# Optimization experiments

Hardware: AMD Instinct MI355X
Metric: run time of the kernel (lower is better)

## Reference

```python
import jax, jax.numpy as jnp
import numpy as np

# Model dims
B, S, H = 1, 1024, 2048
NH, NKV, DH = 32, 8, 64
G = NH // NKV            # GQA group size
E, K, I = 8, 2, 2048     # experts, top_k, intermediate
ALPHA, LIMIT = 1.702, 7.0
EPS = 1e-5
SCALE = DH ** -0.5


def rmsnorm(x, g):
    return x * jax.lax.rsqrt(jnp.mean(x * x, axis=-1, keepdims=True) + EPS) * g


def setup_inputs() -> dict:
    key = jax.random.key(0)
    ks = jax.random.split(key, 24)
    w = lambda k, shp: jax.random.normal(k, shp, dtype=jnp.float32) * 0.02
    causal = jnp.where(jnp.tril(jnp.ones((S, S), dtype=bool)), 0.0, -1e9).astype(jnp.float32)
    return {
        "hidden_states": jax.random.normal(ks[0], (B, S, H), dtype=jnp.float32),
        "attention_bias": causal[None, None, :, :],           # [1,1,S,S]
        "ln1_g": jnp.ones((H,), jnp.float32),
        "ln2_g": jnp.ones((H,), jnp.float32),
        "Wq": w(ks[1], (NH * DH, H)),  "bq": w(ks[2], (NH * DH,)),
        "Wk": w(ks[3], (NKV * DH, H)), "bk": w(ks[4], (NKV * DH,)),
        "Wv": w(ks[5], (NKV * DH, H)), "bv": w(ks[6], (NKV * DH,)),
        "Wo": w(ks[7], (H, NH * DH)),  "bo": w(ks[8], (H,)),
        "sinks": w(ks[9], (NH,)),
        "router_w": w(ks[10], (E, H)), "router_b": w(ks[11], (E,)),
        "We_gate": w(ks[12], (E, I, H)), "be_gate": w(ks[13], (E, I)),
        "We_up":   w(ks[14], (E, I, H)), "be_up":   w(ks[15], (E, I)),
        "We_down": w(ks[16], (E, H, I)), "be_down": w(ks[17], (E, H)),
    }


def reference(hidden_states, attention_bias, ln1_g, ln2_g,
              Wq, bq, Wk, bk, Wv, bv, Wo, bo, sinks,
              router_w, router_b,
              We_gate, be_gate, We_up, be_up, We_down, be_down):
    x = hidden_states
    # ---- pre-norm sink attention ----
    xn = rmsnorm(x, ln1_g)
    q = (xn @ Wq.T + bq).reshape(B, S, NH, DH).transpose(0, 2, 1, 3)    # [B,NH,S,DH]
    k = (xn @ Wk.T + bk).reshape(B, S, NKV, DH).transpose(0, 2, 1, 3)   # [B,NKV,S,DH]
    v = (xn @ Wv.T + bv).reshape(B, S, NKV, DH).transpose(0, 2, 1, 3)
    # GQA: replicate each kv head G times consecutively (repeat_kv)
    k = jnp.repeat(k, G, axis=1)
    v = jnp.repeat(v, G, axis=1)
    scores = jnp.einsum('bhqd,bhkd->bhqk', q, k) * SCALE + attention_bias  # [B,NH,S,S]
    sink_col = jnp.broadcast_to(sinks.reshape(1, NH, 1, 1), (B, NH, S, 1))
    combined = jnp.concatenate([scores, sink_col], axis=-1)               # [B,NH,S,S+1]
    probs = jax.nn.softmax(combined, axis=-1)[..., :-1]                   # drop sink
    attn = jnp.einsum('bhqk,bhkd->bhqd', probs, v)
    attn = attn.transpose(0, 2, 1, 3).reshape(B, S, NH * DH)
    h = x + (attn @ Wo.T + bo)
    # ---- pre-norm MoE FFN ----
    hn = rmsnorm(h, ln2_g)
    router_logits = hn @ router_w.T + router_b                            # [B,S,E]
    rw, sel = jax.lax.top_k(router_logits, K)
    rw = jax.nn.softmax(rw, axis=-1)                                      # [B,S,K]
    # dense per-expert MLP over all tokens (matches the exported loop)
    gate = jnp.einsum('bsh,eih->bsei', hn, We_gate) + be_gate             # [B,S,E,I]
    up = jnp.einsum('bsh,eih->bsei', hn, We_up) + be_up
    gate_c = jnp.minimum(gate, LIMIT)
    up_c = jnp.clip(up, -LIMIT, LIMIT)
    glu = gate_c * jax.nn.sigmoid(ALPHA * gate_c)
    gated = (up_c + 1.0) * glu
    down = jnp.einsum('bsei,ehi->bseh', gated, We_down) + be_down         # [B,S,E,H]
    # per-token expert weight: sum_k rw * (sel == e)
    wts = jnp.sum(rw[..., None] * (sel[..., None] == jnp.arange(E)), axis=2)  # [B,S,E]
    moe = jnp.einsum('bseh,bse->bsh', down, wts)
    return h + moe
```

## Files before the change

### kernel.cpp

```cpp
#include <hip/hip_runtime.h>
#include <hip/hip_bf16.h>

#define HD 2048
#define SEQ 1024
#define NHEAD 32
#define NKVH 8
#define DHEAD 64
#define NEXP 8
#define INTER 2048
#define SCALE 0.125f
#define ALPHA 1.702f
#define LIMIT 7.0f

typedef __attribute__((ext_vector_type(8))) short short8;
typedef __attribute__((ext_vector_type(4))) short short4v;
typedef __attribute__((ext_vector_type(4))) float f32x4;

__device__ __forceinline__ unsigned short f2bf(float f) {
  union { float f; unsigned u; } v; v.f = f;
  unsigned r = v.u + 0x7fffu + ((v.u >> 16) & 1u);
  return (unsigned short)(r >> 16);
}
__device__ __forceinline__ float bf2f(unsigned short h) {
  union { unsigned u; float f; } v; v.u = ((unsigned)h) << 16; return v.f;
}
__device__ __forceinline__ void split2(float f, unsigned short& hi, unsigned short& lo) {
  hi = f2bf(f);
  lo = f2bf(f - bf2f(hi));
}

__device__ __forceinline__ f32x4 mfma32(short8 a, short8 b, f32x4 c) {
  return __builtin_amdgcn_mfma_f32_16x16x32_bf16(a, b, c, 0, 0, 0);
}

__device__ __forceinline__ void gl_lds16(const float* g, float* l) {
  __builtin_amdgcn_global_load_lds(
      (const __attribute__((address_space(1))) unsigned int*)g,
      (__attribute__((address_space(3))) unsigned int*)l, 16, 0, 0);
}

__global__ __launch_bounds__(256) void rmsnorm_split_kernel(
    const float* __restrict__ x, const float* __restrict__ gamma,
    unsigned short* __restrict__ oh, unsigned short* __restrict__ ol) {
  int row = blockIdx.x, tid = threadIdx.x;
  const float* xr = x + (size_t)row * HD;
  float v[8];
#pragma unroll
  for (int i = 0; i < 8; ++i) v[i] = xr[tid * 8 + i];
  float ss = 0.f;
#pragma unroll
  for (int i = 0; i < 8; ++i) ss += v[i] * v[i];
#pragma unroll
  for (int off = 32; off; off >>= 1) ss += __shfl_xor(ss, off, 64);
  __shared__ float wss[4];
  if ((tid & 63) == 0) wss[tid >> 6] = ss;
  __syncthreads();
  float rs = rsqrtf((wss[0] + wss[1] + wss[2] + wss[3]) * (1.0f / HD) + 1e-5f);
  short8 vh, vl;
#pragma unroll
  for (int i = 0; i < 8; ++i) {
    float val = v[i] * rs * gamma[tid * 8 + i];
    unsigned short h, lo;
    split2(val, h, lo);
    vh[i] = (short)h;
    vl[i] = (short)lo;
  }
  *(short8*)(oh + (size_t)row * HD + tid * 8) = vh;
  *(short8*)(ol + (size_t)row * HD + tid * 8) = vl;
}

__global__ __launch_bounds__(256) void rmsnorm_plain_kernel(
    const float* __restrict__ x, const float* __restrict__ gamma,
    unsigned short* __restrict__ out) {
  int row = blockIdx.x, tid = threadIdx.x;
  const float* xr = x + (size_t)row * HD;
  float v[8];
#pragma unroll
  for (int i = 0; i < 8; ++i) v[i] = xr[tid * 8 + i];
  float ss = 0.f;
#pragma unroll
  for (int i = 0; i < 8; ++i) ss += v[i] * v[i];
#pragma unroll
  for (int off = 32; off; off >>= 1) ss += __shfl_xor(ss, off, 64);
  __shared__ float wss[4];
  if ((tid & 63) == 0) wss[tid >> 6] = ss;
  __syncthreads();
  float rs = rsqrtf((wss[0] + wss[1] + wss[2] + wss[3]) * (1.0f / HD) + 1e-5f);
  short8 o;
#pragma unroll
  for (int i = 0; i < 8; ++i) o[i] = (short)f2bf(v[i] * rs * gamma[tid * 8 + i]);
  *(short8*)(out + (size_t)row * HD + tid * 8) = o;
}

template <int MT, int NS, bool SPLIT, int EPI>
__global__ __launch_bounds__(512) void gemm_gl(
    const unsigned short* __restrict__ Ah, const unsigned short* __restrict__ Al,
    int ldA,
    const float* __restrict__ W0, const float* __restrict__ W1,
    const float* __restrict__ W2,
    const float* __restrict__ b0, const float* __restrict__ b1,
    const float* __restrict__ b2,
    const float* __restrict__ resid,
    const int* __restrict__ counts, const int* __restrict__ arows,
    const int* __restrict__ orows,
    unsigned short* __restrict__ oh0, unsigned short* __restrict__ ol0,
    unsigned short* __restrict__ oh1, unsigned short* __restrict__ ol1,
    unsigned short* __restrict__ oh2, unsigned short* __restrict__ ol2,
    float* __restrict__ f0, float* __restrict__ f1,
    int M, int Kd) {
  constexpr int MG = MT * 16 * 8;
  constexpr int NR = NS * 16;
  constexpr int RPW = NR / 8;
  constexpr int NI = RPW / 4;
  __shared__ __align__(16) float lw[2][NR][64];
  int tid = threadIdx.x, l = tid & 63, w = tid >> 6;
  int g = l >> 4, q = l & 15;
  int n0 = blockIdx.x * NR;

  const float* Wb;
  const float* bias;
  int nloc = n0, e = 0, mat = 0;
  if constexpr (EPI == 0) {
    if (n0 < NHEAD * DHEAD) {
      Wb = W0; bias = b0;
    } else if (n0 < NHEAD * DHEAD + NKVH * DHEAD) {
      Wb = W1; bias = b1; nloc = n0 - NHEAD * DHEAD;
    } else {
      Wb = W2; bias = b2; nloc = n0 - (NHEAD * DHEAD + NKVH * DHEAD);
    }
  } else if constexpr (EPI == 1) {
    Wb = W0; bias = b0;
  } else if constexpr (EPI == 2) {
    e = blockIdx.z >> 1;
    mat = blockIdx.z & 1;
    Wb = (mat ? W1 : W0) + (size_t)e * INTER * HD;
    bias = (mat ? b1 : b0) + (size_t)e * INTER;
  } else {
    e = blockIdx.z;
    Wb = W0 + (size_t)e * HD * INTER;
    bias = b0 + (size_t)e * HD;
  }
  int cnt = (EPI >= 2) ? counts[e] : M;

  const float* sptr[NI];
  float* sdst0[NI];
  float* sdst1[NI];
#pragma unroll
  for (int j = 0; j < NI; ++j) {
    int r = RPW * w + 4 * j + (l >> 4);
    int gs = ((l & 15) ^ (r & 7)) * 4;
    sptr[j] = Wb + (size_t)(nloc + r) * Kd + gs;
    sdst0[j] = &lw[0][RPW * w + 4 * j][0];
    sdst1[j] = &lw[1][RPW * w + 4 * j][0];
  }
  auto stage = [&](int buf, int kc) {
#pragma unroll
    for (int j = 0; j < NI; ++j)
      gl_lds16(sptr[j] + kc, buf ? sdst1[j] : sdst0[j]);
  };

  int mstart = (EPI <= 1) ? blockIdx.y : 0;
  int mstep = (EPI <= 1) ? gridDim.y : 1;

  for (int mg = mstart; mg * MG < cnt; mg += mstep) {
    int mb = mg * MG + w * (MT * 16);
    const unsigned short* ap[MT];
    const unsigned short* apl[MT];
#pragma unroll
    for (int mt = 0; mt < MT; ++mt) {
      int mm = min(mb + mt * 16 + q, cnt - 1);
      int ar = (EPI >= 2) ? arows[e * SEQ + mm] : mm;
      ap[mt] = Ah + (size_t)ar * ldA + 8 * g;
      if constexpr (SPLIT) apl[mt] = Al + (size_t)ar * ldA + 8 * g;
    }
    f32x4 acc[MT][NS];
#pragma unroll
    for (int mt = 0; mt < MT; ++mt)
#pragma unroll
      for (int ns = 0; ns < NS; ++ns) acc[mt][ns] = (f32x4){0.f, 0.f, 0.f, 0.f};

    stage(0, 0);
    short8 ab[2][MT], abl[2][MT];
#pragma unroll
    for (int mt = 0; mt < MT; ++mt) {
      ab[0][mt] = *(const short8*)(ap[mt]);
      ab[1][mt] = *(const short8*)(ap[mt] + 32);
      if constexpr (SPLIT) {
        abl[0][mt] = *(const short8*)(apl[mt]);
        abl[1][mt] = *(const short8*)(apl[mt] + 32);
      }
    }
    __syncthreads();

    int nc = Kd / 64;
    for (int c = 0; c < nc; ++c) {
      int u = c & 1;
      if (c + 1 < nc) stage(u ^ 1, (c + 1) * 64);
#pragma unroll
      for (int kh = 0; kh < 2; ++kh) {
        short8 acur[MT], acl[MT];
#pragma unroll
        for (int mt = 0; mt < MT; ++mt) {
          acur[mt] = ab[kh][mt];
          if constexpr (SPLIT) acl[mt] = abl[kh][mt];
        }
        int kn = c * 64 + kh * 32 + 64;
        if (kn < Kd) {
#pragma unroll
          for (int mt = 0; mt < MT; ++mt) {
            ab[kh][mt] = *(const short8*)(ap[mt] + kn);
            if constexpr (SPLIT) abl[kh][mt] = *(const short8*)(apl[mt] + kn);
          }
        }
        short8 wh[NS], wl[NS];
#pragma unroll
        for (int ns = 0; ns < NS; ++ns) {
          int row = ns * 16 + q;
          int r7 = q & 7;
          int i0 = ((kh * 8 + g * 2) ^ r7) * 16;
          int i1 = ((kh * 8 + g * 2 + 1) ^ r7) * 16;
          const char* base = (const char*)&lw[u][row][0];
          float4 v0 = *(const float4*)(base + i0);
          float4 v1 = *(const float4*)(base + i1);
          float vv[8] = {v0.x, v0.y, v0.z, v0.w, v1.x, v1.y, v1.z, v1.w};
#pragma unroll
          for (int jj = 0; jj < 8; ++jj) {
            if constexpr (SPLIT) {
              unsigned short h, lo;
              split2(vv[jj], h, lo);
              wh[ns][jj] = (short)h;
              wl[ns][jj] = (short)lo;
            } else {
              wh[ns][jj] = (short)f2bf(vv[jj]);
            }
          }
        }
#pragma unroll
        for (int mt = 0; mt < MT; ++mt)
#pragma unroll
          for (int ns = 0; ns < NS; ++ns) {
            acc[mt][ns] = mfma32(acur[mt], wh[ns], acc[mt][ns]);
            if constexpr (SPLIT) {
              acc[mt][ns] = mfma32(acur[mt], wl[ns], acc[mt][ns]);
              acc[mt][ns] = mfma32(acl[mt], wh[ns], acc[mt][ns]);
            }
          }
      }
      __syncthreads();
    }
#pragma unroll
    for (int ns = 0; ns < NS; ++ns) {
      int ncol = nloc + ns * 16 + q;
      float bs = bias[ncol];
#pragma unroll
      for (int mt = 0; mt < MT; ++mt) {
#pragma unroll
        for (int r = 0; r < 4; ++r) {
          int mr = mb + mt * 16 + 4 * g + r;
          float val = acc[mt][ns][r] + bs;
          if constexpr (EPI == 0) {
            unsigned short h, lo;
            split2(val, h, lo);
            if (n0 < NHEAD * DHEAD) {
              oh0[(size_t)mr * (NHEAD * DHEAD) + ncol] = h;
              ol0[(size_t)mr * (NHEAD * DHEAD) + ncol] = lo;
            } else if (n0 < NHEAD * DHEAD + NKVH * DHEAD) {
              oh1[(size_t)mr * (NKVH * DHEAD) + ncol] = h;
              ol1[(size_t)mr * (NKVH * DHEAD) + ncol] = lo;
            } else {
              oh2[(size_t)ncol * SEQ + mr] = h;
              ol2[(size_t)ncol * SEQ + mr] = lo;
            }
          } else if constexpr (EPI == 1) {
            f0[(size_t)mr * HD + ncol] = val + resid[(size_t)mr * HD + ncol];
          } else if constexpr (EPI == 2) {
            if (mr < cnt) {
              int slot = orows[e * SEQ + mr];
              (mat ? f1 : f0)[(size_t)slot * INTER + ncol] = val;
            }
          } else {
            if (mr < cnt) {
              int slot = orows[e * SEQ + mr];
              f0[(size_t)slot * HD + ncol] = val;
            }
          }
        }
      }
    }
  }
}

__global__ __launch_bounds__(256) void attn_kernel(
    const unsigned short* __restrict__ Qh, const unsigned short* __restrict__ Ql,
    const unsigned short* __restrict__ Kh, const unsigned short* __restrict__ Kl,
    const unsigned short* __restrict__ Vh, const unsigned short* __restrict__ Vl,
    const float* __restrict__ sinks, unsigned short* __restrict__ outh,
    unsigned short* __restrict__ outl) {
  __shared__ __align__(16) unsigned short pbuf[4][2][16][40];
  int l = threadIdx.x & 63, widx = threadIdx.x >> 6;
  int wid = blockIdx.x * 4 + widx;
  int head = wid >> 6, qt = wid & 63;
  int q0 = qt * 16;
  int g = l >> 4, q = l & 15;
  int kvh = head >> 2;
  size_t qoff = (size_t)(q0 + q) * (NHEAD * DHEAD) + head * DHEAD + 8 * g;
  short8 qh0 = *(const short8*)(Qh + qoff);
  short8 qh1 = *(const short8*)(Qh + qoff + 32);
  short8 ql0 = *(const short8*)(Ql + qoff);
  short8 ql1 = *(const short8*)(Ql + qoff + 32);
  float m = sinks[head];
  float lsum = 1.0f;
  f32x4 o[4] = {{0, 0, 0, 0}, {0, 0, 0, 0}, {0, 0, 0, 0}, {0, 0, 0, 0}};
  int qglob = q0 + q;
  for (int kt = 0; kt <= qt; kt += 2) {
    bool hasB = (kt + 1) <= qt;
    size_t koff = (size_t)(kt * 16 + q) * (NKVH * DHEAD) + kvh * DHEAD + 8 * g;
    f32x4 stA = {0, 0, 0, 0};
    {
      short8 kh0 = *(const short8*)(Kh + koff);
      short8 kh1 = *(const short8*)(Kh + koff + 32);
      short8 kl0 = *(const short8*)(Kl + koff);
      short8 kl1 = *(const short8*)(Kl + koff + 32);
      stA = mfma32(kh0, qh0, stA);
      stA = mfma32(kh0, ql0, stA);
      stA = mfma32(kl0, qh0, stA);
      stA = mfma32(kh1, qh1, stA);
      stA = mfma32(kh1, ql1, stA);
      stA = mfma32(kl1, qh1, stA);
    }
    f32x4 stB = {0, 0, 0, 0};
    if (hasB) {
      size_t koff2 = koff + (size_t)16 * (NKVH * DHEAD);
      short8 kh0 = *(const short8*)(Kh + koff2);
      short8 kh1 = *(const short8*)(Kh + koff2 + 32);
      short8 kl0 = *(const short8*)(Kl + koff2);
      short8 kl1 = *(const short8*)(Kl + koff2 + 32);
      stB = mfma32(kh0, qh0, stB);
      stB = mfma32(kh0, ql0, stB);
      stB = mfma32(kl0, qh0, stB);
      stB = mfma32(kh1, qh1, stB);
      stB = mfma32(kh1, ql1, stB);
      stB = mfma32(kl1, qh1, stB);
    }
    float sA[4], sB[4];
#pragma unroll
    for (int r = 0; r < 4; ++r) {
      int keyA = kt * 16 + 4 * g + r;
      sA[r] = (keyA <= qglob) ? stA[r] * SCALE : -1e30f;
      sB[r] = (hasB && keyA + 16 <= qglob) ? stB[r] * SCALE : -1e30f;
    }
    float mt = fmaxf(fmaxf(fmaxf(sA[0], sA[1]), fmaxf(sA[2], sA[3])),
                     fmaxf(fmaxf(sB[0], sB[1]), fmaxf(sB[2], sB[3])));
    mt = fmaxf(mt, __shfl_xor(mt, 16, 64));
    mt = fmaxf(mt, __shfl_xor(mt, 32, 64));
    float mnew = fmaxf(m, mt);
    float corr = __expf(m - mnew);
    float pA[4], pB[4];
    float rsum = 0.f;
#pragma unroll
    for (int r = 0; r < 4; ++r) {
      pA[r] = __expf(sA[r] - mnew);
      pB[r] = __expf(sB[r] - mnew);
      rsum += pA[r] + pB[r];
    }
    rsum += __shfl_xor(rsum, 16, 64);
    rsum += __shfl_xor(rsum, 32, 64);
    lsum = lsum * corr + rsum;
    m = mnew;
#pragma unroll
    for (int dt = 0; dt < 4; ++dt)
#pragma unroll
      for (int r = 0; r < 4; ++r) o[dt][r] *= corr;
    unsigned short ph[8], pl[8];
#pragma unroll
    for (int r = 0; r < 4; ++r) {
      split2(pA[r], ph[r], pl[r]);
      split2(pB[r], ph[4 + r], pl[4 + r]);
    }
    short4v wAh = {(short)ph[0], (short)ph[1], (short)ph[2], (short)ph[3]};
    short4v wBh = {(short)ph[4], (short)ph[5], (short)ph[6], (short)ph[7]};
    short4v wAl = {(short)pl[0], (short)pl[1], (short)pl[2], (short)pl[3]};
    short4v wBl = {(short)pl[4], (short)pl[5], (short)pl[6], (short)pl[7]};
    *(short4v*)&pbuf[widx][0][q][4 * g] = wAh;
    *(short4v*)&pbuf[widx][0][q][16 + 4 * g] = wBh;
    *(short4v*)&pbuf[widx][1][q][4 * g] = wAl;
    *(short4v*)&pbuf[widx][1][q][16 + 4 * g] = wBl;
    asm volatile("s_waitcnt lgkmcnt(0)" ::: "memory");
    short8 pbh = *(const short8*)&pbuf[widx][0][q][8 * g];
    short8 pbl = *(const short8*)&pbuf[widx][1][q][8 * g];
    size_t vbase = (size_t)(kvh * DHEAD) * SEQ + kt * 16 + 8 * g;
#pragma unroll
    for (int dt = 0; dt < 4; ++dt) {
      size_t voff = vbase + (size_t)(dt * 16 + q) * SEQ;
      short8 vh8 = *(const short8*)(Vh + voff);
      short8 vl8 = *(const short8*)(Vl + voff);
      o[dt] = mfma32(vh8, pbh, o[dt]);
      o[dt] = mfma32(vh8, pbl, o[dt]);
      o[dt] = mfma32(vl8, pbh, o[dt]);
    }
  }
  float inv = 1.0f / lsum;
#pragma unroll
  for (int dt = 0; dt < 4; ++dt)
#pragma unroll
    for (int r = 0; r < 4; ++r) {
      float val = o[dt][r] * inv;
      unsigned short h, lo;
      split2(val, h, lo);
      size_t idx = (size_t)qglob * (NHEAD * DHEAD) + head * DHEAD + dt * 16 + 4 * g + r;
      outh[idx] = h;
      outl[idx] = lo;
    }
}

__global__ __launch_bounds__(64) void router_kernel(
    const float* __restrict__ h, const float* __restrict__ gamma,
    const float* __restrict__ rw, const float* __restrict__ rb,
    float* __restrict__ wsel, int* __restrict__ counts,
    int* __restrict__ lists, int* __restrict__ slotof) {
  int t = blockIdx.x;
  int l = threadIdx.x;
  const float* hr = h + (size_t)t * HD;
  double ss = 0.0;
  for (int i = l; i < HD; i += 64) {
    double x = (double)hr[i];
    ss += x * x;
  }
#pragma unroll
  for (int off = 32; off; off >>= 1) ss += __shfl_xor(ss, off, 64);
  double rs = rsqrt(ss * (1.0 / HD) + 1e-5);
  double acc[NEXP];
#pragma unroll
  for (int e = 0; e < NEXP; ++e) acc[e] = 0.0;
  for (int i = l; i < HD; i += 64) {
    double xh = (double)hr[i] * rs * (double)gamma[i];
#pragma unroll
    for (int e = 0; e < NEXP; ++e) acc[e] += xh * (double)rw[e * HD + i];
  }
#pragma unroll
  for (int e = 0; e < NEXP; ++e)
#pragma unroll
    for (int off = 32; off; off >>= 1) acc[e] += __shfl_xor(acc[e], off, 64);
  if (l == 0) {
    double lg[NEXP];
#pragma unroll
    for (int e = 0; e < NEXP; ++e) lg[e] = acc[e] + (double)rb[e];
    int e0 = 0;
#pragma unroll
    for (int e = 1; e < NEXP; ++e)
      if (lg[e] > lg[e0]) e0 = e;
    int e1 = -1;
#pragma unroll
    for (int e = 0; e < NEXP; ++e)
      if (e != e0 && (e1 < 0 || lg[e] > lg[e1])) e1 = e;
    double d = exp(lg[e1] - lg[e0]);
    float p0 = (float)(1.0 / (1.0 + d)), p1 = (float)(d / (1.0 + d));
    wsel[2 * t] = p0;
    wsel[2 * t + 1] = p1;
    int s0 = atomicAdd(&counts[e0], 1);
    lists[e0 * SEQ + s0] = t;
    slotof[e0 * SEQ + s0] = 2 * t;
    int s1 = atomicAdd(&counts[e1], 1);
    lists[e1 * SEQ + s1] = t;
    slotof[e1 * SEQ + s1] = 2 * t + 1;
  }
}

__global__ __launch_bounds__(256) void act_kernel(
    const float* __restrict__ rg, const float* __restrict__ ru,
    unsigned short* __restrict__ gated) {
  size_t base = (size_t)blockIdx.x * INTER + threadIdx.x * 8;
  float4 g0 = *(const float4*)(rg + base);
  float4 g1 = *(const float4*)(rg + base + 4);
  float4 u0 = *(const float4*)(ru + base);
  float4 u1 = *(const float4*)(ru + base + 4);
  float gv[8] = {g0.x, g0.y, g0.z, g0.w, g1.x, g1.y, g1.z, g1.w};
  float uv[8] = {u0.x, u0.y, u0.z, u0.w, u1.x, u1.y, u1.z, u1.w};
  short8 o;
#pragma unroll
  for (int j = 0; j < 8; ++j) {
    float gc = fminf(gv[j], LIMIT);
    float uc = fminf(fmaxf(uv[j], -LIMIT), LIMIT);
    float glu = gc / (1.f + __expf(-ALPHA * gc));
    o[j] = (short)f2bf((uc + 1.f) * glu);
  }
  *(short8*)(gated + base) = o;
}

__global__ __launch_bounds__(256) void reduce_kernel(
    const float* __restrict__ hbuf, const float* __restrict__ scr,
    const float* __restrict__ wsel, float* __restrict__ out) {
  int t = blockIdx.x;
  int c = threadIdx.x * 8;
  float w0 = wsel[2 * t], w1 = wsel[2 * t + 1];
  size_t hb = (size_t)t * HD + c;
  size_t s0 = (size_t)(2 * t) * HD + c;
  size_t s1 = (size_t)(2 * t + 1) * HD + c;
#pragma unroll
  for (int j = 0; j < 2; ++j) {
    float4 hv = *(const float4*)(hbuf + hb + 4 * j);
    float4 a = *(const float4*)(scr + s0 + 4 * j);
    float4 b = *(const float4*)(scr + s1 + 4 * j);
    float4 r;
    r.x = hv.x + w0 * a.x + w1 * b.x;
    r.y = hv.y + w0 * a.y + w1 * b.y;
    r.z = hv.z + w0 * a.z + w1 * b.z;
    r.w = hv.w + w0 * a.w + w1 * b.w;
    *(float4*)(out + hb + 4 * j) = r;
  }
}

extern "C" void kernel_launch(void* const* d_in, const int* in_sizes, int n_in,
                              void* d_out, int out_size, void* d_ws,
                              size_t ws_size, hipStream_t stream) {
  const float* x = (const float*)d_in[0];
  const float* ln1 = (const float*)d_in[2];
  const float* ln2 = (const float*)d_in[3];
  const float* Wq = (const float*)d_in[4];
  const float* bq = (const float*)d_in[5];
  const float* Wk = (const float*)d_in[6];
  const float* bk = (const float*)d_in[7];
  const float* Wv = (const float*)d_in[8];
  const float* bv = (const float*)d_in[9];
  const float* Wo = (const float*)d_in[10];
  const float* bo = (const float*)d_in[11];
  const float* sinks = (const float*)d_in[12];
  const float* rw = (const float*)d_in[13];
  const float* rb = (const float*)d_in[14];
  const float* Wg = (const float*)d_in[15];
  const float* bg = (const float*)d_in[16];
  const float* Wu = (const float*)d_in[17];
  const float* bu = (const float*)d_in[18];
  const float* Wd = (const float*)d_in[19];
  const float* bd = (const float*)d_in[20];
  float* out = (float*)d_out;

  char* ws = (char*)d_ws;
  size_t off = 0;
  auto alloc = [&](size_t bytes) {
    void* p = ws + off;
    off += (bytes + 255) & ~(size_t)255;
    return p;
  };
  unsigned short* xnh = (unsigned short*)alloc((size_t)SEQ * HD * 2);
  unsigned short* xnl = (unsigned short*)alloc((size_t)SEQ * HD * 2);
  unsigned short* qbh = (unsigned short*)alloc((size_t)SEQ * NHEAD * DHEAD * 2);
  unsigned short* qbl = (unsigned short*)alloc((size_t)SEQ * NHEAD * DHEAD * 2);
  unsigned short* kbh = (unsigned short*)alloc((size_t)SEQ * NKVH * DHEAD * 2);
  unsigned short* kbl = (unsigned short*)alloc((size_t)SEQ * NKVH * DHEAD * 2);
  unsigned short* vth = (unsigned short*)alloc((size_t)NKVH * DHEAD * SEQ * 2);
  unsigned short* vtl = (unsigned short*)alloc((size_t)NKVH * DHEAD * SEQ * 2);
  unsigned short* ath = (unsigned short*)alloc((size_t)SEQ * NHEAD * DHEAD * 2);
  unsigned short* atl = (unsigned short*)alloc((size_t)SEQ * NHEAD * DHEAD * 2);
  float* hbuf = (float*)alloc((size_t)SEQ * HD * 4);
  unsigned short* hn = (unsigned short*)alloc((size_t)SEQ * HD * 2);
  float* wsel = (float*)alloc((size_t)SEQ * 2 * 4);
  int* counts = (int*)alloc(NEXP * 4);
  int* lists = (int*)alloc((size_t)NEXP * SEQ * 4);
  int* slotof = (int*)alloc((size_t)NEXP * SEQ * 4);
  float* rawg = (float*)alloc((size_t)2 * SEQ * INTER * 4);
  float* rawu = (float*)alloc((size_t)2 * SEQ * INTER * 4);
  unsigned short* gated = (unsigned short*)alloc((size_t)2 * SEQ * INTER * 2);
  float* scr = rawg;
  (void)ws_size;
  (void)off;

  rmsnorm_split_kernel<<<SEQ, 256, 0, stream>>>(x, ln1, xnh, xnl);
  gemm_gl<2, 2, true, 0><<<dim3(96, 4, 1), 512, 0, stream>>>(
      xnh, xnl, HD, Wq, Wk, Wv, bq, bk, bv, nullptr, nullptr, nullptr, nullptr,
      qbh, qbl, kbh, kbl, vth, vtl, nullptr, nullptr, SEQ, HD);
  attn_kernel<<<NHEAD * 64 / 4, 256, 0, stream>>>(qbh, qbl, kbh, kbl, vth, vtl,
                                                  sinks, ath, atl);
  gemm_gl<2, 2, true, 1><<<dim3(64, 4, 1), 512, 0, stream>>>(
      ath, atl, NHEAD * DHEAD, Wo, nullptr, nullptr, bo, nullptr, nullptr, x,
      nullptr, nullptr, nullptr, nullptr, nullptr, nullptr, nullptr, nullptr,
      nullptr, hbuf, nullptr, SEQ, NHEAD * DHEAD);
  rmsnorm_plain_kernel<<<SEQ, 256, 0, stream>>>(hbuf, ln2, hn);
  hipMemsetAsync(counts, 0, NEXP * sizeof(int), stream);
  router_kernel<<<SEQ, 64, 0, stream>>>(hbuf, ln2, rw, rb, wsel, counts, lists,
                                        slotof);
  gemm_gl<3, 4, false, 2><<<dim3(32, 1, 16), 512, 0, stream>>>(
      hn, nullptr, HD, Wg, Wu, nullptr, bg, bu, nullptr, nullptr, counts, lists,
      slotof, nullptr, nullptr, nullptr, nullptr, nullptr, nullptr, rawg, rawu,
      SEQ, HD);
  act_kernel<<<2 * SEQ, 256, 0, stream>>>(rawg, rawu, gated);
  gemm_gl<3, 2, false, 3><<<dim3(64, 1, 8), 512, 0, stream>>>(
      gated, nullptr, INTER, Wd, nullptr, nullptr, bd, nullptr, nullptr,
      nullptr, counts, slotof, slotof, nullptr, nullptr, nullptr, nullptr,
      nullptr, nullptr, scr, nullptr, SEQ, INTER);
  reduce_kernel<<<SEQ, 256, 0, stream>>>(hbuf, scr, wsel, out);
}
```

Baseline: 643.3 us.

## Convert staged fp32 weights to bf16 once per tile in shared memory

```diff
diff --git a/kernel.cpp b/kernel.cpp
--- a/kernel.cpp
+++ b/kernel.cpp
@@ -112,7 +112,9 @@
   constexpr int NR = NS * 16;
   constexpr int RPW = NR / 8;
   constexpr int NI = RPW / 4;
-  __shared__ __align__(16) float lw[2][NR][64];
+  constexpr int NPL = SPLIT ? 2 : 1;
+  __shared__ __align__(16) float f32b[2][NR][64];
+  __shared__ __align__(16) unsigned short bfb[2][NPL][NR][72];
   int tid = threadIdx.x, l = tid & 63, w = tid >> 6;
   int g = l >> 4, q = l & 15;
   int n0 = blockIdx.x * NR;
@@ -150,13 +152,53 @@
     int r = RPW * w + 4 * j + (l >> 4);
     int gs = ((l & 15) ^ (r & 7)) * 4;
     sptr[j] = Wb + (size_t)(nloc + r) * Kd + gs;
-    sdst0[j] = &lw[0][RPW * w + 4 * j][0];
-    sdst1[j] = &lw[1][RPW * w + 4 * j][0];
+    sdst0[j] = &f32b[0][RPW * w + 4 * j][0];
+    sdst1[j] = &f32b[1][RPW * w + 4 * j][0];
   }
   auto stage = [&](int buf, int kc) {
 #pragma unroll
     for (int j = 0; j < NI; ++j)
       gl_lds16(sptr[j] + kc, buf ? sdst1[j] : sdst0[j]);
+  };
+  auto convert = [&](int p) {
+    if constexpr (NR == 64) {
+      int crow = tid >> 3, cj = tid & 7, r7 = crow & 7;
+      float4 a = *(const float4*)&f32b[p][crow][((2 * cj) ^ r7) * 4];
+      float4 b = *(const float4*)&f32b[p][crow][((2 * cj + 1) ^ r7) * 4];
+      float vv[8] = {a.x, a.y, a.z, a.w, b.x, b.y, b.z, b.w};
+      short8 hh, ll;
+#pragma unroll
+      for (int j = 0; j < 8; ++j) {
+        if constexpr (SPLIT) {
+          unsigned short h, lo;
+          split2(vv[j], h, lo);
+          hh[j] = (short)h;
+          ll[j] = (short)lo;
+        } else {
+          hh[j] = (short)f2bf(vv[j]);
+        }
+      }
+      *(short8*)&bfb[p][0][crow][8 * cj] = hh;
+      if constexpr (SPLIT) *(short8*)&bfb[p][NPL - 1][crow][8 * cj] = ll;
+    } else {
+      int crow = tid >> 4, cs = tid & 15, r7 = crow & 7;
+      float4 a = *(const float4*)&f32b[p][crow][(cs ^ r7) * 4];
+      float vv[4] = {a.x, a.y, a.z, a.w};
+      short4v hh, ll;
+#pragma unroll
+      for (int j = 0; j < 4; ++j) {
+        if constexpr (SPLIT) {
+          unsigned short h, lo;
+          split2(vv[j], h, lo);
+          hh[j] = (short)h;
+          ll[j] = (short)lo;
+        } else {
+          hh[j] = (short)f2bf(vv[j]);
+        }
+      }
+      *(short4v*)&bfb[p][0][crow][4 * cs] = hh;
+      if constexpr (SPLIT) *(short4v*)&bfb[p][NPL - 1][crow][4 * cs] = ll;
+    }
   };
 
   int mstart = (EPI <= 1) ? blockIdx.y : 0;
@@ -191,6 +233,8 @@
       }
     }
     __syncthreads();
+    convert(0);
+    __syncthreads();
 
     int nc = Kd / 64;
     for (int c = 0; c < nc; ++c) {
@@ -215,25 +259,9 @@
         short8 wh[NS], wl[NS];
 #pragma unroll
         for (int ns = 0; ns < NS; ++ns) {
-          int row = ns * 16 + q;
-          int r7 = q & 7;
-          int i0 = ((kh * 8 + g * 2) ^ r7) * 16;
-          int i1 = ((kh * 8 + g * 2 + 1) ^ r7) * 16;
-          const char* base = (const char*)&lw[u][row][0];
-          float4 v0 = *(const float4*)(base + i0);
-          float4 v1 = *(const float4*)(base + i1);
-          float vv[8] = {v0.x, v0.y, v0.z, v0.w, v1.x, v1.y, v1.z, v1.w};
-#pragma unroll
-          for (int jj = 0; jj < 8; ++jj) {
-            if constexpr (SPLIT) {
-              unsigned short h, lo;
-              split2(vv[jj], h, lo);
-              wh[ns][jj] = (short)h;
-              wl[ns][jj] = (short)lo;
-            } else {
-              wh[ns][jj] = (short)f2bf(vv[jj]);
-            }
-          }
+          wh[ns] = *(const short8*)&bfb[u][0][ns * 16 + q][kh * 32 + 8 * g];
+          if constexpr (SPLIT)
+            wl[ns] = *(const short8*)&bfb[u][NPL - 1][ns * 16 + q][kh * 32 + 8 * g];
         }
 #pragma unroll
         for (int mt = 0; mt < MT; ++mt)
@@ -247,6 +275,10 @@
           }
       }
       __syncthreads();
+      if (c + 1 < nc) {
+        convert(u ^ 1);
+        __syncthreads();
+      }
     }
 #pragma unroll
     for (int ns = 0; ns < NS; ++ns) {
@@ -287,6 +319,7 @@
         }
       }
     }
+    if (mg + mstep < (cnt + MG - 1) / MG || true) __syncthreads();
   }
 }
 
```

After: 621.7 us. -3.4%, faster.
